# Optimization experiments

Hardware: AMD Instinct MI355X
Metric: run time of the kernel (lower is better)

Reference implementation:

```python
import jax, jax.numpy as jnp
import numpy as np
import math

B, S, D, H, TD = 256, 200, 64, 512, 8


def setup_inputs():
    key = jax.random.key(0)
    ks = jax.random.split(key, 12)
    sd, sh, so = 1.0 / math.sqrt(D), 1.0 / math.sqrt(H), 1.0 / math.sqrt(H + TD)
    return dict(
        x=jax.random.normal(ks[0], (B, S, D), jnp.float32),
        a=jax.random.normal(ks[3], (B, TD), jnp.float32),
        t=jnp.cumsum(jax.random.uniform(ks[2], (B, S), jnp.float32), axis=1),
        mask=(jax.random.uniform(ks[1], (B, S, D)) < 0.8).astype(jnp.float32),
        w_dg_x=jax.random.normal(ks[4], (D,), jnp.float32) * sd,
        b_dg_x=jnp.zeros((D,), jnp.float32),
        W_dg_h=jax.random.normal(ks[5], (H, D), jnp.float32) * sd,
        b_dg_h=jnp.zeros((H,), jnp.float32),
        W=jax.random.normal(ks[6], (3 * H, D), jnp.float32) * sd,
        U=jax.random.normal(ks[7], (3 * H, H), jnp.float32) * sh,
        V=jax.random.normal(ks[8], (3 * H, D), jnp.float32) * sd,
        b=jnp.zeros((3 * H,), jnp.float32),
        attn_v=jnp.ones((H,), jnp.float32),
        W_out=jax.random.normal(ks[9], (H, H + TD), jnp.float32) * so,
        b_out=jnp.zeros((H,), jnp.float32),
    )


def reference(x, a, t, mask, w_dg_x, b_dg_x, W_dg_h, b_dg_h, W, U, V, b, attn_v, W_out, b_out):
    # ---- GRU-D preprocessing: per-feature time gaps delta ----
    x_tm = jnp.transpose(x, (1, 0, 2))    # (S,B,D) time-major
    m_tm = jnp.transpose(mask, (1, 0, 2))
    dt = jnp.diff(t, axis=1, prepend=t[:, :1])      # (B,S), dt[0]=0
    dt_tm = jnp.transpose(dt)[:, :, None]           # (S,B,1)
    # delta[i] = dt[i] + (1 - mask[i-1]) * delta[i-1]; ones at step 0 -> delta[0]=0
    m_prev = jnp.concatenate([jnp.ones((1,) + m_tm.shape[1:], m_tm.dtype), m_tm[:-1]], axis=0)

    def delta_step(d, inp):
        dt_i, mp_i = inp
        d = dt_i + (1.0 - mp_i) * d
        return d, d

    _, delta_tm = jax.lax.scan(delta_step, jnp.zeros((B, D), x.dtype), (dt_tm, m_prev))

    # empirical mean of observed values for imputation
    x_mean = (mask * x).sum((0, 1)) / jnp.maximum(mask.sum((0, 1)), 1.0)  # (D,)

    Wz, Wr, Wh = W[:H], W[H:2 * H], W[2 * H:]
    Uz, Ur, Uh = U[:H], U[H:2 * H], U[2 * H:]
    Vz, Vr, Vh = V[:H], V[H:2 * H], V[2 * H:]
    bz, br, bh = b[:H], b[H:2 * H], b[2 * H:]

    def cell(carry, inp):
        h, x_last = carry
        x_i, m_i, d_i = inp                                        # (B,D) each
        gamma_x = jnp.exp(-jax.nn.relu(w_dg_x * d_i + b_dg_x))     # (B,D) input decay
        gamma_h = jnp.exp(-jax.nn.relu(d_i @ W_dg_h.T + b_dg_h))   # (B,H) hidden decay
        x_hat = m_i * x_i + (1.0 - m_i) * (gamma_x * x_last + (1.0 - gamma_x) * x_mean)
        h_dec = gamma_h * h
        z = jax.nn.sigmoid(x_hat @ Wz.T + h_dec @ Uz.T + m_i @ Vz.T + bz)
        r = jax.nn.sigmoid(x_hat @ Wr.T + h_dec @ Ur.T + m_i @ Vr.T + br)
        h_til = jnp.tanh(x_hat @ Wh.T + (r * h_dec) @ Uh.T + m_i @ Vh.T + bh)
        h_new = (1.0 - z) * h_dec + z * h_til
        x_last_new = m_i * x_i + (1.0 - m_i) * x_last
        return (h_new, x_last_new), h_new

    init = (jnp.zeros((B, H), x.dtype), jnp.zeros((B, D), x.dtype))
    _, h_all = jax.lax.scan(cell, init, (x_tm, m_tm, delta_tm))    # (S,B,H)

    # ---- attention pooling over time (softmax along seq dim, as in torch dim=0) ----
    score = (h_all @ attn_v) / math.sqrt(H)        # (S,B)
    w_attn = jax.nn.softmax(score, axis=0)
    attn_h = (h_all * w_attn[..., None]).sum(0)    # (B,H)

    # ---- treatment head ----
    return jnp.concatenate([attn_h, a], axis=1) @ W_out.T + b_out  # (B,H)
```

## Files before the change

### kernel.cpp

```cpp
#include <hip/hip_runtime.h>
#include <hip/hip_bf16.h>
#include <stdint.h>


typedef unsigned short u16;
typedef unsigned int   u32;
typedef unsigned long long u64;
typedef short bfrag  __attribute__((ext_vector_type(8)));
typedef u16   u16x8  __attribute__((ext_vector_type(8)));
typedef float f32x4  __attribute__((ext_vector_type(4)));

#define NB 256
#define NS 200
#define ND 64
#define NH 512

union UQ  { u16x8 h; bfrag s; u64 u[2]; uint4 q; };
union UF2 { float f[2]; u64 u; };

__device__ __forceinline__ float b2f(u16 v){ union { float f; u32 u; } c; c.u = ((u32)v) << 16; return c.f; }
__device__ __forceinline__ u16 f2b(float f){ union { float f; u32 u; } c; c.f = f; u32 r = c.u + 0x7FFFu + ((c.u >> 16) & 1u); return (u16)(r >> 16); }
__device__ __forceinline__ float sigm(float x){ return 1.f / (1.f + __expf(-x)); }
__device__ __forceinline__ float tanh_f(float x){ return 1.f - 2.f / (1.f + __expf(2.f * x)); }

__device__ __forceinline__ u64 cload64(const void* p){
  return __hip_atomic_load((const u64*)p, __ATOMIC_RELAXED, __HIP_MEMORY_SCOPE_AGENT);
}
__device__ __forceinline__ void cstore64(void* p, u64 v){
  __hip_atomic_store((u64*)p, v, __ATOMIC_RELAXED, __HIP_MEMORY_SCOPE_AGENT);
}
__device__ __forceinline__ void load8f_c(const float* p, float* f){
  UF2 w;
  w.u = cload64(p + 0); f[0]=w.f[0]; f[1]=w.f[1];
  w.u = cload64(p + 2); f[2]=w.f[0]; f[3]=w.f[1];
  w.u = cload64(p + 4); f[4]=w.f[0]; f[5]=w.f[1];
  w.u = cload64(p + 6); f[6]=w.f[0]; f[7]=w.f[1];
}
__device__ __forceinline__ void store8f_c(float* p, const float* f){
  UF2 w;
  w.f[0]=f[0]; w.f[1]=f[1]; cstore64(p + 0, w.u);
  w.f[0]=f[2]; w.f[1]=f[3]; cstore64(p + 2, w.u);
  w.f[0]=f[4]; w.f[1]=f[5]; cstore64(p + 4, w.u);
  w.f[0]=f[6]; w.f[1]=f[7]; cstore64(p + 6, w.u);
}
__device__ __forceinline__ void spin_ge(u32* f, u32 tgt){
  while (__hip_atomic_load(f, __ATOMIC_RELAXED, __HIP_MEMORY_SCOPE_AGENT) < tgt)
    __builtin_amdgcn_s_sleep(2);
}
__device__ __forceinline__ bfrag ldfrag(const float* src){
  f32x4 lo = *(const f32x4*)src;
  f32x4 hi = *(const f32x4*)(src + 4);
  UQ z;
  z.h[0]=f2b(lo[0]); z.h[1]=f2b(lo[1]); z.h[2]=f2b(lo[2]); z.h[3]=f2b(lo[3]);
  z.h[4]=f2b(hi[0]); z.h[5]=f2b(hi[1]); z.h[6]=f2b(hi[2]); z.h[7]=f2b(hi[3]);
  return z.s;
}


__global__ void transpose_k(const float* __restrict__ Wout, float* __restrict__ WT){
  int i = blockIdx.x * 256 + threadIdx.x;
  if (i < 520 * 512) { int k = i >> 9, ho = i & 511; WT[i] = Wout[ho * 520 + k]; }
}

__global__ void mean1_k(const float* __restrict__ x, const float* __restrict__ mask,
                        float* __restrict__ PX, float* __restrict__ PM){
  int s = blockIdx.x, tid = threadIdx.x;
  __shared__ float lx[256], lm[256];
  float xa = 0.f, ma = 0.f;
  for (int i = tid; i < NB * ND; i += 256) {
    int b = i >> 6, d = i & 63;
    size_t ix = ((size_t)b * NS + s) * 64 + d;
    float m = mask[ix];
    xa += m * x[ix]; ma += m;
  }
  lx[tid] = xa; lm[tid] = ma;
  __syncthreads();
  if (tid < 64) {
    PX[(size_t)s * 64 + tid] = lx[tid] + lx[tid + 64] + lx[tid + 128] + lx[tid + 192];
    PM[(size_t)s * 64 + tid] = lm[tid] + lm[tid + 64] + lm[tid + 128] + lm[tid + 192];
  }
}

__global__ void mean2_k(const float* __restrict__ PX, const float* __restrict__ PM,
                        float* __restrict__ XMEAN){
  int d = threadIdx.x;
  float sx = 0.f, sm = 0.f;
  for (int s = 0; s < NS; ++s){ sx += PX[s * 64 + d]; sm += PM[s * 64 + d]; }
  XMEAN[d] = sx / fmaxf(sm, 1.f);
}

__global__ void prep_k(const float* __restrict__ x, const float* __restrict__ mask,
                       const float* __restrict__ tc, const float* __restrict__ wdgx,
                       const float* __restrict__ bdgx, const float* __restrict__ XMEAN,
                       u16* __restrict__ XHAT, u16* __restrict__ MASKB, u16* __restrict__ DELTA){
  int g = blockIdx.x * 256 + threadIdx.x;
  int b = g >> 6, d = g & 63;
  float xmean = XMEAN[d], wx = wdgx[d], bx = bdgx[d];
  float xl = 0.f, del = 0.f, tprev = 0.f, mprev = 1.f;
  for (int s = 0; s < NS; ++s){
    float tv = tc[b * NS + s];
    float dtv = (s == 0) ? 0.f : (tv - tprev);
    tprev = tv;
    del = dtv + (1.f - mprev) * del;
    size_t ix = ((size_t)b * NS + s) * 64 + d;
    float m = mask[ix], xv = x[ix];
    float gx = __expf(-fmaxf(0.f, wx * del + bx));
    float xh = m * xv + (1.f - m) * (gx * xl + (1.f - gx) * xmean);
    size_t ox = ((size_t)s * NB + b) * 64 + d;
    XHAT[ox] = f2b(xh); MASKB[ox] = f2b(m); DELTA[ox] = f2b(del);
    xl = m * xv + (1.f - m) * xl;
    mprev = m;
  }
}

__global__ __launch_bounds__(256, 1) void grud_rnn(
    const float* __restrict__ Um, const float* __restrict__ Wm, const float* __restrict__ Vm,
    const float* __restrict__ bv, const float* __restrict__ Wdg, const float* __restrict__ bdg,
    const u16* __restrict__ XHAT, const u16* __restrict__ MASKB, const u16* __restrict__ DELTA,
    float* __restrict__ HDEC, u16* __restrict__ RHD, float* __restrict__ ZB,
    float* __restrict__ SHP, u16* __restrict__ HALL, u32* done1, u32* done2)
{
  const int tid = threadIdx.x, lane = tid & 63, wid = tid >> 6, bid = blockIdx.x;
  __shared__ u16 panel[80 * 16 * 8];
  __shared__ u16 dpanel[8 * 16 * 8];
  __shared__ float xpose[4][528];
  float* xp = xpose[wid];
  const int r = lane >> 2, cb = (lane & 3) * 8;
  const int krow = lane >> 4;

  if (bid < 192) {
    const int rb = bid / 12, sg = bid % 12;
    const int type = (sg < 4) ? 0 : ((sg < 8) ? 1 : 2);
    const int st = sg * 4 + wid;
    const int cglob = st * 32;
    const int m0 = rb * 16;
    const int c0 = cglob + (lane & 15);

    bfrag Bf[20][2];
    #pragma unroll
    for (int kk = 0; kk < 20; ++kk) {
      if (!(type == 2 && kk < 16)) {
        const int k0 = kk * 32 + krow * 8;
        #pragma unroll
        for (int t2 = 0; t2 < 2; ++t2) {
          const int c = c0 + t2 * 16;
          const float* src;
          if (k0 < 512)      src = Um + (size_t)c * 512 + k0;
          else if (k0 < 576) src = Wm + (size_t)c * 64 + (k0 - 512);
          else               src = Vm + (size_t)c * 64 + (k0 - 576);
          Bf[kk][t2] = ldfrag(src);
        }
      }
    }
    const float bias0 = bv[c0], bias1 = bv[c0 + 16];

    for (int t = 0; t < NS; ++t) {
      {
        const int isrc = tid >> 7, row = (tid >> 3) & 15, kb8 = tid & 7;
        const u16* sp = (isrc ? MASKB : XHAT) + ((size_t)t * NB + (m0 + row)) * 64 + kb8 * 8;
        uint4 vv = *(const uint4*)sp;
        *(uint4*)&panel[(((isrc ? 72 : 64) + kb8) * 16 + row) * 8] = vv;
      }
      if (tid == 0) spin_ge(done2 + rb * 16, 4u * (u32)t);
      __syncthreads();
      if (type != 2) {
        #pragma unroll
        for (int it = 0; it < 4; ++it) {
          const int c = it * 256 + tid;
          const int row = c >> 6, kb = c & 63;
          float f[8];
          load8f_c(HDEC + (size_t)(m0 + row) * 512 + kb * 8, f);
          UQ pv;
          #pragma unroll
          for (int j = 0; j < 8; ++j) pv.h[j] = f2b(f[j]);
          *(u16x8*)&panel[(kb * 16 + row) * 8] = pv.h;
        }
      }
      __syncthreads();
      f32x4 acc0 = {bias0, bias0, bias0, bias0};
      f32x4 acc1 = {bias1, bias1, bias1, bias1};
      #pragma unroll
      for (int kk = 0; kk < 20; ++kk) {
        if (!(type == 2 && kk < 16)) {
          bfrag a = *(const bfrag*)&panel[((kk * 4 + krow) * 16 + (lane & 15)) * 8];
          acc0 = __builtin_amdgcn_mfma_f32_16x16x32_bf16(a, Bf[kk][0], acc0, 0, 0, 0);
          acc1 = __builtin_amdgcn_mfma_f32_16x16x32_bf16(a, Bf[kk][1], acc1, 0, 0, 0);
        }
      }
      {
        const int r0 = krow * 4, cc = lane & 15;
        #pragma unroll
        for (int j = 0; j < 4; ++j) { xp[(r0 + j) * 33 + cc] = acc0[j]; xp[(r0 + j) * 33 + 16 + cc] = acc1[j]; }
      }
      float s8[8];
      #pragma unroll
      for (int q = 0; q < 8; ++q) s8[q] = xp[r * 33 + cb + q];
      const size_t orow = (size_t)(m0 + r) * 512;
      if (type == 0) {
        float zf[8];
        #pragma unroll
        for (int q = 0; q < 8; ++q) zf[q] = sigm(s8[q]);
        store8f_c(ZB + orow + cglob + cb, zf);
      } else if (type == 1) {
        const int hc = cglob - 512 + cb;
        UQ hv; hv.h = *(const u16x8*)&panel[((hc >> 3) * 16 + r) * 8];
        UQ pv;
        #pragma unroll
        for (int q = 0; q < 8; ++q) pv.h[q] = f2b(sigm(s8[q]) * b2f(hv.h[q]));
        u16* dst = RHD + orow + hc;
        cstore64(dst, pv.u[0]); cstore64(dst + 4, pv.u[1]);
      } else {
        store8f_c(SHP + orow + (cglob - 1024) + cb, s8);
      }
      asm volatile("s_waitcnt vmcnt(0)" ::: "memory");
      __syncthreads();
      if (tid == 0) __hip_atomic_fetch_add(done1 + rb * 16, 1u, __ATOMIC_RELAXED, __HIP_MEMORY_SCOPE_AGENT);
    }
  } else {
    const int b2 = bid - 192;
    const int rb = b2 >> 2, sg = b2 & 3;
    const int st = sg * 4 + wid;
    const int n0 = st * 32;
    const int m0 = rb * 16;
    const int c0 = n0 + (lane & 15);

    bfrag Bh[16][2];
    #pragma unroll
    for (int kk = 0; kk < 16; ++kk) {
      const int k0 = kk * 32 + krow * 8;
      #pragma unroll
      for (int t2 = 0; t2 < 2; ++t2)
        Bh[kk][t2] = ldfrag(Um + (size_t)(1024 + c0 + t2 * 16) * 512 + k0);
    }
    bfrag Bg[2][2];
    #pragma unroll
    for (int kk = 0; kk < 2; ++kk) {
      const int k0 = kk * 32 + krow * 8;
      #pragma unroll
      for (int t2 = 0; t2 < 2; ++t2)
        Bg[kk][t2] = ldfrag(Wdg + (size_t)(c0 + t2 * 16) * 64 + k0);
    }
    const float gb0 = bdg[c0], gb1 = bdg[c0 + 16];

    for (int t = 0; t < NS; ++t) {
      float gam[8] = {0,0,0,0,0,0,0,0};
      if (t < NS - 1) {
        if (tid < 128) {
          const int row = (tid >> 3) & 15, kb8 = tid & 7;
          const u16* sp = DELTA + ((size_t)(t + 1) * NB + (m0 + row)) * 64 + kb8 * 8;
          *(uint4*)&dpanel[(kb8 * 16 + row) * 8] = *(const uint4*)sp;
        }
        __syncthreads();
        f32x4 g0 = {gb0, gb0, gb0, gb0};
        f32x4 g1 = {gb1, gb1, gb1, gb1};
        #pragma unroll
        for (int kk = 0; kk < 2; ++kk) {
          bfrag a = *(const bfrag*)&dpanel[((kk * 4 + krow) * 16 + (lane & 15)) * 8];
          g0 = __builtin_amdgcn_mfma_f32_16x16x32_bf16(a, Bg[kk][0], g0, 0, 0, 0);
          g1 = __builtin_amdgcn_mfma_f32_16x16x32_bf16(a, Bg[kk][1], g1, 0, 0, 0);
        }
        const int r0 = krow * 4, cc = lane & 15;
        #pragma unroll
        for (int j = 0; j < 4; ++j) { xp[(r0 + j) * 33 + cc] = g0[j]; xp[(r0 + j) * 33 + 16 + cc] = g1[j]; }
        #pragma unroll
        for (int q = 0; q < 8; ++q) gam[q] = __expf(-fmaxf(0.f, xp[r * 33 + cb + q]));
      }
      if (tid == 0) spin_ge(done1 + rb * 16, 12u * (u32)(t + 1));
      __syncthreads();
      #pragma unroll
      for (int it = 0; it < 4; ++it) {
        const int c = it * 256 + tid;
        const int row = c >> 6, kb = c & 63;
        const u16* sp = RHD + (size_t)(m0 + row) * 512 + kb * 8;
        UQ pv; pv.u[0] = cload64(sp); pv.u[1] = cload64(sp + 4);
        *(u16x8*)&panel[(kb * 16 + row) * 8] = pv.h;
      }
      __syncthreads();
      f32x4 acc0 = {0.f, 0.f, 0.f, 0.f}, acc1 = {0.f, 0.f, 0.f, 0.f};
      #pragma unroll
      for (int kk = 0; kk < 16; ++kk) {
        bfrag a = *(const bfrag*)&panel[((kk * 4 + krow) * 16 + (lane & 15)) * 8];
        acc0 = __builtin_amdgcn_mfma_f32_16x16x32_bf16(a, Bh[kk][0], acc0, 0, 0, 0);
        acc1 = __builtin_amdgcn_mfma_f32_16x16x32_bf16(a, Bh[kk][1], acc1, 0, 0, 0);
      }
      {
        const int r0 = krow * 4, cc = lane & 15;
        #pragma unroll
        for (int j = 0; j < 4; ++j) { xp[(r0 + j) * 33 + cc] = acc0[j]; xp[(r0 + j) * 33 + 16 + cc] = acc1[j]; }
      }
      const int hc = n0 + cb;
      const size_t orow = (size_t)(m0 + r) * 512;
      float s2[8], shp[8], zz[8], hd[8], hn[8], hdn[8];
      #pragma unroll
      for (int q = 0; q < 8; ++q) s2[q] = xp[r * 33 + cb + q];
      load8f_c(SHP + orow + hc, shp);
      load8f_c(ZB + orow + hc, zz);
      load8f_c(HDEC + orow + hc, hd);
      UQ hw;
      #pragma unroll
      for (int q = 0; q < 8; ++q) {
        float til = tanh_f(shp[q] + s2[q]);
        hn[q] = (1.f - zz[q]) * hd[q] + zz[q] * til;
        hw.h[q] = f2b(hn[q]);
        hdn[q] = gam[q] * hn[q];
      }
      u16* hp = HALL + ((size_t)t * NB + (m0 + r)) * 512 + hc;
      cstore64(hp, hw.u[0]); cstore64(hp + 4, hw.u[1]);
      if (t < NS - 1) store8f_c(HDEC + orow + hc, hdn);
      asm volatile("s_waitcnt vmcnt(0)" ::: "memory");
      __syncthreads();
      if (tid == 0) __hip_atomic_fetch_add(done2 + rb * 16, 1u, __ATOMIC_RELAXED, __HIP_MEMORY_SCOPE_AGENT);
    }
  }
}


__global__ void attn_k(const u16* __restrict__ HALL, const float* __restrict__ av,
                       float* __restrict__ ATTN){
  const int b = blockIdx.x, tid = threadIdx.x, lane = tid & 63, wid = tid >> 6;
  __shared__ float avs[512], wgt[256], red[8];
  for (int i = tid; i < 512; i += 256) avs[i] = av[i];
  __syncthreads();
  float val = -3.0e38f;
  if (tid < NS) {
    const u16* hp = HALL + ((size_t)tid * NB + b) * 512;
    float acc = 0.f;
    for (int h = 0; h < 512; h += 8) {
      UQ w; w.q = *(const uint4*)(hp + h);
      #pragma unroll
      for (int j = 0; j < 8; ++j) acc += b2f(w.h[j]) * avs[h + j];
    }
    val = acc * 0.04419417382415922f;
  }
  float m = val;
  #pragma unroll
  for (int off = 32; off; off >>= 1) m = fmaxf(m, __shfl_xor(m, off, 64));
  if (lane == 0) red[wid] = m;
  __syncthreads();
  m = fmaxf(fmaxf(red[0], red[1]), fmaxf(red[2], red[3]));
  float e = (tid < NS) ? __expf(val - m) : 0.f;
  float sum = e;
  #pragma unroll
  for (int off = 32; off; off >>= 1) sum += __shfl_xor(sum, off, 64);
  if (lane == 0) red[4 + wid] = sum;
  __syncthreads();
  const float ssum = red[4] + red[5] + red[6] + red[7];
  wgt[tid] = e / ssum;
  __syncthreads();
  float a0 = 0.f, a1 = 0.f;
  const int h0 = tid * 2;
  for (int s = 0; s < NS; ++s) {
    float w = wgt[s];
    u32 pr = *(const u32*)(HALL + ((size_t)s * NB + b) * 512 + h0);
    a0 += w * b2f((u16)(pr & 0xFFFFu));
    a1 += w * b2f((u16)(pr >> 16));
  }
  ATTN[(size_t)b * 512 + h0] = a0;
  ATTN[(size_t)b * 512 + h0 + 1] = a1;
}

__global__ void out_k(const float* __restrict__ ATTN, const float* __restrict__ Ain,
                      const float* __restrict__ WT, const float* __restrict__ bout,
                      float* __restrict__ OUT){
  const int b = blockIdx.x, tid = threadIdx.x;
  __shared__ float ah[512], aa[8];
  for (int i = tid; i < 512; i += 256) ah[i] = ATTN[(size_t)b * 512 + i];
  if (tid < 8) aa[tid] = Ain[b * 8 + tid];
  __syncthreads();
  #pragma unroll
  for (int part = 0; part < 2; ++part) {
    const int ho = part * 256 + tid;
    float acc = bout[ho];
    #pragma unroll 8
    for (int k = 0; k < 512; ++k) acc += ah[k] * WT[(size_t)k * 512 + ho];
    #pragma unroll
    for (int k = 0; k < 8; ++k) acc += aa[k] * WT[(size_t)(512 + k) * 512 + ho];
    OUT[(size_t)b * 512 + ho] = acc;
  }
}


extern "C" void kernel_launch(void* const* d_in, const int* in_sizes, int n_in,
                              void* d_out, int out_size, void* d_ws, size_t ws_size,
                              hipStream_t stream) {
  (void)in_sizes; (void)n_in; (void)out_size; (void)ws_size;
  const float* x    = (const float*)d_in[0];
  const float* a_in = (const float*)d_in[1];
  const float* tc   = (const float*)d_in[2];
  const float* mask = (const float*)d_in[3];
  const float* wdgx = (const float*)d_in[4];
  const float* bdgx = (const float*)d_in[5];
  const float* Wdgh = (const float*)d_in[6];
  const float* bdgh = (const float*)d_in[7];
  const float* Wm   = (const float*)d_in[8];
  const float* Um   = (const float*)d_in[9];
  const float* Vm   = (const float*)d_in[10];
  const float* bvv  = (const float*)d_in[11];
  const float* attv = (const float*)d_in[12];
  const float* Wout = (const float*)d_in[13];
  const float* bout = (const float*)d_in[14];

  char* ws = (char*)d_ws;
  size_t o = 0;
  auto al = [&](size_t sz) { size_t r = o; o += (sz + 255) & ~(size_t)255; return r; };
  u32*   flags = (u32*)  (ws + al(4096));
  float* XMEAN = (float*)(ws + al(256));
  float* PX    = (float*)(ws + al((size_t)NS * 64 * 4));
  float* PM    = (float*)(ws + al((size_t)NS * 64 * 4));
  u16*   XHAT  = (u16*)  (ws + al((size_t)NS * NB * 64 * 2));
  u16*   MASKB = (u16*)  (ws + al((size_t)NS * NB * 64 * 2));
  u16*   DELTA = (u16*)  (ws + al((size_t)NS * NB * 64 * 2));
  float* HDEC  = (float*)(ws + al((size_t)NB * NH * 4));
  u16*   RHD   = (u16*)  (ws + al((size_t)NB * NH * 2));
  float* ZB    = (float*)(ws + al((size_t)NB * NH * 4));
  float* SHP   = (float*)(ws + al((size_t)NB * NH * 4));
  u16*   HALL  = (u16*)  (ws + al((size_t)NS * NB * NH * 2));
  float* ATTN  = (float*)(ws + al((size_t)NB * NH * 4));
  float* WT    = (float*)(ws + al((size_t)520 * 512 * 4));
  u32* done1 = flags;
  u32* done2 = flags + 256;

  hipMemsetAsync(flags, 0, 4096, stream);
  hipMemsetAsync(HDEC, 0, (size_t)NB * NH * 4, stream);

  transpose_k<<<(520 * 512 + 255) / 256, 256, 0, stream>>>(Wout, WT);
  mean1_k<<<NS, 256, 0, stream>>>(x, mask, PX, PM);
  mean2_k<<<1, 64, 0, stream>>>(PX, PM, XMEAN);
  prep_k<<<NB * ND / 256, 256, 0, stream>>>(x, mask, tc, wdgx, bdgx, XMEAN, XHAT, MASKB, DELTA);
  grud_rnn<<<256, 256, 0, stream>>>(Um, Wm, Vm, bvv, Wdgh, bdgh, XHAT, MASKB, DELTA,
                                    HDEC, RHD, ZB, SHP, HALL, done1, done2);
  attn_k<<<NB, 256, 0, stream>>>(HALL, attv, ATTN);
  out_k<<<NB, 256, 0, stream>>>(ATTN, a_in, WT, bout, (float*)d_out);
}
```

Before: 2.266 ms.

## Restructure GRU-D recurrence into pipelined hidden, input-projection and decay roles

The persistent RNN kernel is reorganised into 112 blocks per 16-row batch tile with three roles. Four blocks hold all U gate weights and run the recurrent matmuls. Two blocks precompute input and mask projections one step ahead into double-buffered bf16 slots. One block precomputes hidden-decay gammas ahead. Hidden state and r*h exchanges move from fp32 to bf16, and the spin waits now have bounded fuel with an abort flag. out_k is also batched over four rows per block to reuse W_out loads. The aim is to take the non-recurrent matmuls off the serial critical path, at the cost of more fine-grained flag synchronisation per step and a new intra-step barrier between the r and h-tilde phases.

```diff
diff --git a/kernel.cpp b/kernel.cpp
--- a/kernel.cpp
+++ b/kernel.cpp
@@ -15,6 +15,8 @@
 #define ND 64
 #define NH 512
 
+#define MFMA(a,b,c) __builtin_amdgcn_mfma_f32_16x16x32_bf16((a),(b),(c),0,0,0)
+
 union UQ  { u16x8 h; bfrag s; u64 u[2]; uint4 q; };
 union UF2 { float f[2]; u64 u; };
 
@@ -29,23 +31,16 @@
 __device__ __forceinline__ void cstore64(void* p, u64 v){
   __hip_atomic_store((u64*)p, v, __ATOMIC_RELAXED, __HIP_MEMORY_SCOPE_AGENT);
 }
-__device__ __forceinline__ void load8f_c(const float* p, float* f){
-  UF2 w;
-  w.u = cload64(p + 0); f[0]=w.f[0]; f[1]=w.f[1];
-  w.u = cload64(p + 2); f[2]=w.f[0]; f[3]=w.f[1];
-  w.u = cload64(p + 4); f[4]=w.f[0]; f[5]=w.f[1];
-  w.u = cload64(p + 6); f[6]=w.f[0]; f[7]=w.f[1];
-}
-__device__ __forceinline__ void store8f_c(float* p, const float* f){
-  UF2 w;
-  w.f[0]=f[0]; w.f[1]=f[1]; cstore64(p + 0, w.u);
-  w.f[0]=f[2]; w.f[1]=f[3]; cstore64(p + 2, w.u);
-  w.f[0]=f[4]; w.f[1]=f[5]; cstore64(p + 4, w.u);
-  w.f[0]=f[6]; w.f[1]=f[7]; cstore64(p + 6, w.u);
-}
-__device__ __forceinline__ void spin_ge(u32* f, u32 tgt){
-  while (__hip_atomic_load(f, __ATOMIC_RELAXED, __HIP_MEMORY_SCOPE_AGENT) < tgt)
-    __builtin_amdgcn_s_sleep(2);
+__device__ __forceinline__ bool spin_ge(u32* f, u32 tgt){
+  int fuel = 1 << 19;
+  while (__hip_atomic_load(f, __ATOMIC_RELAXED, __HIP_MEMORY_SCOPE_AGENT) < tgt) {
+    __builtin_amdgcn_s_sleep(1);
+    if (--fuel == 0) return false;
+  }
+  return true;
+}
+__device__ __forceinline__ void flag_add(u32* f){
+  __hip_atomic_fetch_add(f, 1u, __ATOMIC_RELAXED, __HIP_MEMORY_SCOPE_AGENT);
 }
 __device__ __forceinline__ bfrag ldfrag(const float* src){
   f32x4 lo = *(const f32x4*)src;
@@ -117,199 +112,242 @@
     const float* __restrict__ Um, const float* __restrict__ Wm, const float* __restrict__ Vm,
     const float* __restrict__ bv, const float* __restrict__ Wdg, const float* __restrict__ bdg,
     const u16* __restrict__ XHAT, const u16* __restrict__ MASKB, const u16* __restrict__ DELTA,
-    float* __restrict__ HDEC, u16* __restrict__ RHD, float* __restrict__ ZB,
-    float* __restrict__ SHP, u16* __restrict__ HALL, u32* done1, u32* done2)
+    u16* __restrict__ HDECB, u16* __restrict__ RHB, u16* __restrict__ XPART,
+    u16* __restrict__ GAMB, u16* __restrict__ HALL, u32* __restrict__ flags)
 {
   const int tid = threadIdx.x, lane = tid & 63, wid = tid >> 6, bid = blockIdx.x;
-  __shared__ u16 panel[80 * 16 * 8];
-  __shared__ u16 dpanel[8 * 16 * 8];
-  __shared__ float xpose[4][528];
-  float* xp = xpose[wid];
-  const int r = lane >> 2, cb = (lane & 3) * 8;
-  const int krow = lane >> 4;
-
-  if (bid < 192) {
-    const int rb = bid / 12, sg = bid % 12;
-    const int type = (sg < 4) ? 0 : ((sg < 8) ? 1 : 2);
-    const int st = sg * 4 + wid;
-    const int cglob = st * 32;
-    const int m0 = rb * 16;
-    const int c0 = cglob + (lane & 15);
-
-    bfrag Bf[20][2];
-    #pragma unroll
-    for (int kk = 0; kk < 20; ++kk) {
-      if (!(type == 2 && kk < 16)) {
-        const int k0 = kk * 32 + krow * 8;
-        #pragma unroll
-        for (int t2 = 0; t2 < 2; ++t2) {
-          const int c = c0 + t2 * 16;
-          const float* src;
-          if (k0 < 512)      src = Um + (size_t)c * 512 + k0;
-          else if (k0 < 576) src = Wm + (size_t)c * 64 + (k0 - 512);
-          else               src = Vm + (size_t)c * 64 + (k0 - 576);
-          Bf[kk][t2] = ldfrag(src);
-        }
-      }
-    }
-    const float bias0 = bv[c0], bias1 = bv[c0 + 16];
-
-    for (int t = 0; t < NS; ++t) {
-      {
-        const int isrc = tid >> 7, row = (tid >> 3) & 15, kb8 = tid & 7;
-        const u16* sp = (isrc ? MASKB : XHAT) + ((size_t)t * NB + (m0 + row)) * 64 + kb8 * 8;
-        uint4 vv = *(const uint4*)sp;
-        *(uint4*)&panel[(((isrc ? 72 : 64) + kb8) * 16 + row) * 8] = vv;
-      }
-      if (tid == 0) spin_ge(done2 + rb * 16, 4u * (u32)t);
-      __syncthreads();
-      if (type != 2) {
-        #pragma unroll
-        for (int it = 0; it < 4; ++it) {
-          const int c = it * 256 + tid;
-          const int row = c >> 6, kb = c & 63;
-          float f[8];
-          load8f_c(HDEC + (size_t)(m0 + row) * 512 + kb * 8, f);
-          UQ pv;
-          #pragma unroll
-          for (int j = 0; j < 8; ++j) pv.h[j] = f2b(f[j]);
-          *(u16x8*)&panel[(kb * 16 + row) * 8] = pv.h;
-        }
-      }
-      __syncthreads();
-      f32x4 acc0 = {bias0, bias0, bias0, bias0};
-      f32x4 acc1 = {bias1, bias1, bias1, bias1};
-      #pragma unroll
-      for (int kk = 0; kk < 20; ++kk) {
-        if (!(type == 2 && kk < 16)) {
-          bfrag a = *(const bfrag*)&panel[((kk * 4 + krow) * 16 + (lane & 15)) * 8];
-          acc0 = __builtin_amdgcn_mfma_f32_16x16x32_bf16(a, Bf[kk][0], acc0, 0, 0, 0);
-          acc1 = __builtin_amdgcn_mfma_f32_16x16x32_bf16(a, Bf[kk][1], acc1, 0, 0, 0);
-        }
-      }
-      {
-        const int r0 = krow * 4, cc = lane & 15;
-        #pragma unroll
-        for (int j = 0; j < 4; ++j) { xp[(r0 + j) * 33 + cc] = acc0[j]; xp[(r0 + j) * 33 + 16 + cc] = acc1[j]; }
-      }
-      float s8[8];
-      #pragma unroll
-      for (int q = 0; q < 8; ++q) s8[q] = xp[r * 33 + cb + q];
-      const size_t orow = (size_t)(m0 + r) * 512;
-      if (type == 0) {
-        float zf[8];
-        #pragma unroll
-        for (int q = 0; q < 8; ++q) zf[q] = sigm(s8[q]);
-        store8f_c(ZB + orow + cglob + cb, zf);
-      } else if (type == 1) {
-        const int hc = cglob - 512 + cb;
-        UQ hv; hv.h = *(const u16x8*)&panel[((hc >> 3) * 16 + r) * 8];
-        UQ pv;
-        #pragma unroll
-        for (int q = 0; q < 8; ++q) pv.h[q] = f2b(sigm(s8[q]) * b2f(hv.h[q]));
-        u16* dst = RHD + orow + hc;
-        cstore64(dst, pv.u[0]); cstore64(dst + 4, pv.u[1]);
-      } else {
-        store8f_c(SHP + orow + (cglob - 1024) + cb, s8);
-      }
-      asm volatile("s_waitcnt vmcnt(0)" ::: "memory");
-      __syncthreads();
-      if (tid == 0) __hip_atomic_fetch_add(done1 + rb * 16, 1u, __ATOMIC_RELAXED, __HIP_MEMORY_SCOPE_AGENT);
-    }
-  } else {
-    const int b2 = bid - 192;
-    const int rb = b2 >> 2, sg = b2 & 3;
-    const int st = sg * 4 + wid;
-    const int n0 = st * 32;
-    const int m0 = rb * 16;
-    const int c0 = n0 + (lane & 15);
-
-    bfrag Bh[16][2];
+  const int rb = bid / 7, role = bid % 7, m0 = rb * 16;
+  const int l16 = lane & 15, krow = lane >> 4, r4 = lane >> 2, cb = (lane & 3) * 8;
+  u32* FH = flags + rb * 128;
+  u32* FR = flags + rb * 128 + 32;
+  u32* FX = flags + rb * 128 + 64;
+  u32* FG = flags + rb * 128 + 96;
+
+  __shared__ u16 hpanel[64 * 16 * 8];
+  __shared__ u16 rhpanel[64 * 16 * 8];
+  __shared__ float xb[4][16 * 33];
+  __shared__ int s_ab;
+  float* xw = xb[wid];
+  const f32x4 Z4 = {0.f, 0.f, 0.f, 0.f};
+  if (tid == 0) s_ab = 0;
+  __syncthreads();
+
+  if (role < 4) {
+    const int c0g = role * 128 + wid * 32;
+    bfrag BUz[16][2], BUr[16][2], BUh[16][2];
     #pragma unroll
     for (int kk = 0; kk < 16; ++kk) {
-      const int k0 = kk * 32 + krow * 8;
-      #pragma unroll
-      for (int t2 = 0; t2 < 2; ++t2)
-        Bh[kk][t2] = ldfrag(Um + (size_t)(1024 + c0 + t2 * 16) * 512 + k0);
-    }
-    bfrag Bg[2][2];
+      #pragma unroll
+      for (int t2 = 0; t2 < 2; ++t2) {
+        const size_t ko = (size_t)(kk * 32 + krow * 8);
+        BUz[kk][t2] = ldfrag(Um + (size_t)(       c0g + t2 * 16 + l16) * 512 + ko);
+        BUr[kk][t2] = ldfrag(Um + (size_t)(512  + c0g + t2 * 16 + l16) * 512 + ko);
+        BUh[kk][t2] = ldfrag(Um + (size_t)(1024 + c0g + t2 * 16 + l16) * 512 + ko);
+      }
+    }
+
+    for (int t = 0; t < NS; ++t) {
+      const int slot = t & 1;
+      if (tid == 0 && t > 0)  { if (!spin_ge(FH, 4u * (u32)t)) s_ab = 1; }
+      if (tid == 64)          { if (!spin_ge(FX, 2u * (u32)(t + 1))) s_ab = 1; }
+      if (tid == 128)         { u32 gt = (t + 1 < NS) ? (u32)(t + 1) : (u32)(NS - 1);
+                                if (!spin_ge(FG, gt)) s_ab = 1; }
+      __syncthreads();
+      if (s_ab) break;
+      const u16* xpb = XPART + (((size_t)slot * 16 + rb) * 16 + r4) * 1536;
+      u64 xz0 = cload64(xpb + c0g + cb),        xz1 = cload64(xpb + c0g + cb + 4);
+      u64 xr0 = cload64(xpb + 512 + c0g + cb),  xr1 = cload64(xpb + 512 + c0g + cb + 4);
+      u64 xh0 = cload64(xpb + 1024 + c0g + cb), xh1 = cload64(xpb + 1024 + c0g + cb + 4);
+      u64 gm0 = 0, gm1 = 0;
+      if (t + 1 < NS) {
+        const u16* gpb = GAMB + (((size_t)((t + 1) & 1) * 16 + rb) * 16 + r4) * 512 + c0g + cb;
+        gm0 = cload64(gpb); gm1 = cload64(gpb + 4);
+      }
+      {
+        const int srow = tid >> 4, sc = (tid & 15) * 32;
+        u16* dp = &hpanel[((sc >> 3) * 16 + srow) * 8];
+        if (t > 0) {
+          const u16* hs = HDECB + (size_t)(m0 + srow) * 512 + sc;
+          u64 a0 = cload64(hs),      a1 = cload64(hs + 4),  a2 = cload64(hs + 8),  a3 = cload64(hs + 12);
+          u64 a4 = cload64(hs + 16), a5 = cload64(hs + 20), a6 = cload64(hs + 24), a7 = cload64(hs + 28);
+          *(u64*)(dp)       = a0; *(u64*)(dp + 4)   = a1;
+          *(u64*)(dp + 128) = a2; *(u64*)(dp + 132) = a3;
+          *(u64*)(dp + 256) = a4; *(u64*)(dp + 260) = a5;
+          *(u64*)(dp + 384) = a6; *(u64*)(dp + 388) = a7;
+        } else {
+          *(u64*)(dp)       = 0; *(u64*)(dp + 4)   = 0;
+          *(u64*)(dp + 128) = 0; *(u64*)(dp + 132) = 0;
+          *(u64*)(dp + 256) = 0; *(u64*)(dp + 260) = 0;
+          *(u64*)(dp + 384) = 0; *(u64*)(dp + 388) = 0;
+        }
+      }
+      __syncthreads();
+      f32x4 ar0 = Z4, ar1 = Z4;
+      #pragma unroll
+      for (int kk = 0; kk < 16; ++kk) {
+        bfrag a = *(const bfrag*)&hpanel[((kk * 4 + krow) * 16 + l16) * 8];
+        ar0 = MFMA(a, BUr[kk][0], ar0); ar1 = MFMA(a, BUr[kk][1], ar1);
+      }
+      #pragma unroll
+      for (int j = 0; j < 4; ++j) { xw[(krow*4+j)*33 + l16] = ar0[j]; xw[(krow*4+j)*33 + 16 + l16] = ar1[j]; }
+      UQ xru; xru.u[0] = xr0; xru.u[1] = xr1;
+      UQ hdu; hdu.h = *(const u16x8*)&hpanel[(((c0g + cb) >> 3) * 16 + r4) * 8];
+      UQ rhv;
+      #pragma unroll
+      for (int q = 0; q < 8; ++q) {
+        float rv = sigm(b2f(xru.h[q]) + xw[r4 * 33 + cb + q]);
+        rhv.h[q] = f2b(rv * b2f(hdu.h[q]));
+      }
+      { u16* dst = RHB + (size_t)(m0 + r4) * 512 + c0g + cb;
+        cstore64(dst, rhv.u[0]); cstore64(dst + 4, rhv.u[1]); }
+      asm volatile("s_waitcnt vmcnt(0)" ::: "memory");
+      __syncthreads();
+      if (tid == 0) flag_add(FR);
+      f32x4 az0 = Z4, az1 = Z4;
+      #pragma unroll
+      for (int kk = 0; kk < 16; ++kk) {
+        bfrag a = *(const bfrag*)&hpanel[((kk * 4 + krow) * 16 + l16) * 8];
+        az0 = MFMA(a, BUz[kk][0], az0); az1 = MFMA(a, BUz[kk][1], az1);
+      }
+      #pragma unroll
+      for (int j = 0; j < 4; ++j) { xw[(krow*4+j)*33 + l16] = az0[j]; xw[(krow*4+j)*33 + 16 + l16] = az1[j]; }
+      UQ xzu; xzu.u[0] = xz0; xzu.u[1] = xz1;
+      float zz8[8];
+      #pragma unroll
+      for (int q = 0; q < 8; ++q) zz8[q] = sigm(b2f(xzu.h[q]) + xw[r4 * 33 + cb + q]);
+      if (tid == 0) { if (!spin_ge(FR, 4u * (u32)(t + 1))) s_ab = 1; }
+      __syncthreads();
+      if (s_ab) break;
+      {
+        const int srow = tid >> 4, sc = (tid & 15) * 32;
+        const u16* rs = RHB + (size_t)(m0 + srow) * 512 + sc;
+        u64 a0 = cload64(rs),      a1 = cload64(rs + 4),  a2 = cload64(rs + 8),  a3 = cload64(rs + 12);
+        u64 a4 = cload64(rs + 16), a5 = cload64(rs + 20), a6 = cload64(rs + 24), a7 = cload64(rs + 28);
+        u16* dp = &rhpanel[((sc >> 3) * 16 + srow) * 8];
+        *(u64*)(dp)       = a0; *(u64*)(dp + 4)   = a1;
+        *(u64*)(dp + 128) = a2; *(u64*)(dp + 132) = a3;
+        *(u64*)(dp + 256) = a4; *(u64*)(dp + 260) = a5;
+        *(u64*)(dp + 384) = a6; *(u64*)(dp + 388) = a7;
+      }
+      __syncthreads();
+      f32x4 ah0 = Z4, ah1 = Z4;
+      #pragma unroll
+      for (int kk = 0; kk < 16; ++kk) {
+        bfrag a = *(const bfrag*)&rhpanel[((kk * 4 + krow) * 16 + l16) * 8];
+        ah0 = MFMA(a, BUh[kk][0], ah0); ah1 = MFMA(a, BUh[kk][1], ah1);
+      }
+      #pragma unroll
+      for (int j = 0; j < 4; ++j) { xw[(krow*4+j)*33 + l16] = ah0[j]; xw[(krow*4+j)*33 + 16 + l16] = ah1[j]; }
+      UQ xhu; xhu.u[0] = xh0; xhu.u[1] = xh1;
+      UQ hwv; float hn8[8];
+      #pragma unroll
+      for (int q = 0; q < 8; ++q) {
+        float til = tanh_f(b2f(xhu.h[q]) + xw[r4 * 33 + cb + q]);
+        float hdq = b2f(hdu.h[q]);
+        float hv = (1.f - zz8[q]) * hdq + zz8[q] * til;
+        hn8[q] = hv; hwv.h[q] = f2b(hv);
+      }
+      if (t + 1 < NS) {
+        UQ gmu; gmu.u[0] = gm0; gmu.u[1] = gm1;
+        UQ hdn;
+        #pragma unroll
+        for (int q = 0; q < 8; ++q) hdn.h[q] = f2b(b2f(gmu.h[q]) * hn8[q]);
+        u16* dp2 = HDECB + (size_t)(m0 + r4) * 512 + c0g + cb;
+        cstore64(dp2, hdn.u[0]); cstore64(dp2 + 4, hdn.u[1]);
+      }
+      asm volatile("s_waitcnt vmcnt(0)" ::: "memory");
+      __syncthreads();
+      if (tid == 0) flag_add(FH);
+      *(uint4*)(HALL + ((size_t)t * NB + m0 + r4) * 512 + c0g + cb) = hwv.q;
+    }
+  } else if (role < 6) {
+    const int p = role - 4;
+    const int wbase = p * 768 + wid * 192;
+    bfrag BW[12][2], BV2[12][2];
     #pragma unroll
-    for (int kk = 0; kk < 2; ++kk) {
-      const int k0 = kk * 32 + krow * 8;
-      #pragma unroll
-      for (int t2 = 0; t2 < 2; ++t2)
-        Bg[kk][t2] = ldfrag(Wdg + (size_t)(c0 + t2 * 16) * 64 + k0);
-    }
-    const float gb0 = bdg[c0], gb1 = bdg[c0 + 16];
+    for (int ct = 0; ct < 12; ++ct)
+      #pragma unroll
+      for (int kx = 0; kx < 2; ++kx) {
+        BW[ct][kx]  = ldfrag(Wm + (size_t)(wbase + ct * 16 + l16) * 64 + kx * 32 + krow * 8);
+        BV2[ct][kx] = ldfrag(Vm + (size_t)(wbase + ct * 16 + l16) * 64 + kx * 32 + krow * 8);
+      }
+    float bias6[6][8];
+    #pragma unroll
+    for (int grp = 0; grp < 6; ++grp)
+      #pragma unroll
+      for (int q = 0; q < 8; ++q) bias6[grp][q] = bv[wbase + grp * 32 + cb + q];
 
     for (int t = 0; t < NS; ++t) {
-      float gam[8] = {0,0,0,0,0,0,0,0};
-      if (t < NS - 1) {
-        if (tid < 128) {
-          const int row = (tid >> 3) & 15, kb8 = tid & 7;
-          const u16* sp = DELTA + ((size_t)(t + 1) * NB + (m0 + row)) * 64 + kb8 * 8;
-          *(uint4*)&dpanel[(kb8 * 16 + row) * 8] = *(const uint4*)sp;
+      if (tid == 0 && t >= 2) { if (!spin_ge(FH, 4u * (u32)(t - 1))) s_ab = 1; }
+      { const int kb = tid >> 4, row = tid & 15;
+        const u16* sp = (kb < 8 ? XHAT : MASKB) + ((size_t)t * NB + m0 + row) * 64 + (kb & 7) * 8;
+        *(uint4*)&hpanel[(kb * 16 + row) * 8] = *(const uint4*)sp; }
+      __syncthreads();
+      if (s_ab) break;
+      u16* orow_ = XPART + (((size_t)(t & 1) * 16 + rb) * 16 + r4) * 1536 + wbase;
+      #pragma unroll
+      for (int grp = 0; grp < 6; ++grp) {
+        f32x4 ac0 = Z4, ac1 = Z4;
+        #pragma unroll
+        for (int kx = 0; kx < 2; ++kx) {
+          bfrag ax = *(const bfrag*)&hpanel[((kx * 4 + krow) * 16 + l16) * 8];
+          ac0 = MFMA(ax, BW[grp*2][kx], ac0); ac1 = MFMA(ax, BW[grp*2+1][kx], ac1);
+          bfrag am = *(const bfrag*)&hpanel[((8 + kx * 4 + krow) * 16 + l16) * 8];
+          ac0 = MFMA(am, BV2[grp*2][kx], ac0); ac1 = MFMA(am, BV2[grp*2+1][kx], ac1);
         }
-        __syncthreads();
-        f32x4 g0 = {gb0, gb0, gb0, gb0};
-        f32x4 g1 = {gb1, gb1, gb1, gb1};
-        #pragma unroll
-        for (int kk = 0; kk < 2; ++kk) {
-          bfrag a = *(const bfrag*)&dpanel[((kk * 4 + krow) * 16 + (lane & 15)) * 8];
-          g0 = __builtin_amdgcn_mfma_f32_16x16x32_bf16(a, Bg[kk][0], g0, 0, 0, 0);
-          g1 = __builtin_amdgcn_mfma_f32_16x16x32_bf16(a, Bg[kk][1], g1, 0, 0, 0);
+        #pragma unroll
+        for (int j = 0; j < 4; ++j) { xw[(krow*4+j)*33 + l16] = ac0[j]; xw[(krow*4+j)*33 + 16 + l16] = ac1[j]; }
+        UQ ov;
+        #pragma unroll
+        for (int q = 0; q < 8; ++q) ov.h[q] = f2b(xw[r4 * 33 + cb + q] + bias6[grp][q]);
+        cstore64(orow_ + grp * 32 + cb, ov.u[0]); cstore64(orow_ + grp * 32 + cb + 4, ov.u[1]);
+      }
+      asm volatile("s_waitcnt vmcnt(0)" ::: "memory");
+      __syncthreads();
+      if (tid == 0) flag_add(FX);
+    }
+  } else {
+    bfrag BG[8][2];
+    #pragma unroll
+    for (int ct = 0; ct < 8; ++ct)
+      #pragma unroll
+      for (int kx = 0; kx < 2; ++kx)
+        BG[ct][kx] = ldfrag(Wdg + (size_t)(wid * 128 + ct * 16 + l16) * 64 + kx * 32 + krow * 8);
+    float gb4[4][8];
+    #pragma unroll
+    for (int grp = 0; grp < 4; ++grp)
+      #pragma unroll
+      for (int q = 0; q < 8; ++q) gb4[grp][q] = bdg[wid * 128 + grp * 32 + cb + q];
+
+    for (int tt = 1; tt < NS; ++tt) {
+      if (tid == 0 && tt >= 3) { if (!spin_ge(FH, 4u * (u32)(tt - 2))) s_ab = 1; }
+      if (tid < 128) {
+        const int kb = tid >> 4, row = tid & 15;
+        const u16* sp = DELTA + ((size_t)tt * NB + m0 + row) * 64 + kb * 8;
+        *(uint4*)&hpanel[(kb * 16 + row) * 8] = *(const uint4*)sp;
+      }
+      __syncthreads();
+      if (s_ab) break;
+      u16* orow_ = GAMB + (((size_t)(tt & 1) * 16 + rb) * 16 + r4) * 512 + wid * 128;
+      #pragma unroll
+      for (int grp = 0; grp < 4; ++grp) {
+        f32x4 ac0 = Z4, ac1 = Z4;
+        #pragma unroll
+        for (int kx = 0; kx < 2; ++kx) {
+          bfrag a = *(const bfrag*)&hpanel[((kx * 4 + krow) * 16 + l16) * 8];
+          ac0 = MFMA(a, BG[grp*2][kx], ac0); ac1 = MFMA(a, BG[grp*2+1][kx], ac1);
         }
-        const int r0 = krow * 4, cc = lane & 15;
-        #pragma unroll
-        for (int j = 0; j < 4; ++j) { xp[(r0 + j) * 33 + cc] = g0[j]; xp[(r0 + j) * 33 + 16 + cc] = g1[j]; }
-        #pragma unroll
-        for (int q = 0; q < 8; ++q) gam[q] = __expf(-fmaxf(0.f, xp[r * 33 + cb + q]));
-      }
-      if (tid == 0) spin_ge(done1 + rb * 16, 12u * (u32)(t + 1));
-      __syncthreads();
-      #pragma unroll
-      for (int it = 0; it < 4; ++it) {
-        const int c = it * 256 + tid;
-        const int row = c >> 6, kb = c & 63;
-        const u16* sp = RHD + (size_t)(m0 + row) * 512 + kb * 8;
-        UQ pv; pv.u[0] = cload64(sp); pv.u[1] = cload64(sp + 4);
-        *(u16x8*)&panel[(kb * 16 + row) * 8] = pv.h;
-      }
-      __syncthreads();
-      f32x4 acc0 = {0.f, 0.f, 0.f, 0.f}, acc1 = {0.f, 0.f, 0.f, 0.f};
-      #pragma unroll
-      for (int kk = 0; kk < 16; ++kk) {
-        bfrag a = *(const bfrag*)&panel[((kk * 4 + krow) * 16 + (lane & 15)) * 8];
-        acc0 = __builtin_amdgcn_mfma_f32_16x16x32_bf16(a, Bh[kk][0], acc0, 0, 0, 0);
-        acc1 = __builtin_amdgcn_mfma_f32_16x16x32_bf16(a, Bh[kk][1], acc1, 0, 0, 0);
-      }
-      {
-        const int r0 = krow * 4, cc = lane & 15;
-        #pragma unroll
-        for (int j = 0; j < 4; ++j) { xp[(r0 + j) * 33 + cc] = acc0[j]; xp[(r0 + j) * 33 + 16 + cc] = acc1[j]; }
-      }
-      const int hc = n0 + cb;
-      const size_t orow = (size_t)(m0 + r) * 512;
-      float s2[8], shp[8], zz[8], hd[8], hn[8], hdn[8];
-      #pragma unroll
-      for (int q = 0; q < 8; ++q) s2[q] = xp[r * 33 + cb + q];
-      load8f_c(SHP + orow + hc, shp);
-      load8f_c(ZB + orow + hc, zz);
-      load8f_c(HDEC + orow + hc, hd);
-      UQ hw;
-      #pragma unroll
-      for (int q = 0; q < 8; ++q) {
-        float til = tanh_f(shp[q] + s2[q]);
-        hn[q] = (1.f - zz[q]) * hd[q] + zz[q] * til;
-        hw.h[q] = f2b(hn[q]);
-        hdn[q] = gam[q] * hn[q];
-      }
-      u16* hp = HALL + ((size_t)t * NB + (m0 + r)) * 512 + hc;
-      cstore64(hp, hw.u[0]); cstore64(hp + 4, hw.u[1]);
-      if (t < NS - 1) store8f_c(HDEC + orow + hc, hdn);
+        #pragma unroll
+        for (int j = 0; j < 4; ++j) { xw[(krow*4+j)*33 + l16] = ac0[j]; xw[(krow*4+j)*33 + 16 + l16] = ac1[j]; }
+        UQ ov;
+        #pragma unroll
+        for (int q = 0; q < 8; ++q)
+          ov.h[q] = f2b(__expf(-fmaxf(0.f, xw[r4 * 33 + cb + q] + gb4[grp][q])));
+        cstore64(orow_ + grp * 32 + cb, ov.u[0]); cstore64(orow_ + grp * 32 + cb + 4, ov.u[1]);
+      }
       asm volatile("s_waitcnt vmcnt(0)" ::: "memory");
       __syncthreads();
-      if (tid == 0) __hip_atomic_fetch_add(done2 + rb * 16, 1u, __ATOMIC_RELAXED, __HIP_MEMORY_SCOPE_AGENT);
+      if (tid == 0) flag_add(FG);
     }
   }
 }
@@ -362,20 +400,26 @@
 __global__ void out_k(const float* __restrict__ ATTN, const float* __restrict__ Ain,
                       const float* __restrict__ WT, const float* __restrict__ bout,
                       float* __restrict__ OUT){
-  const int b = blockIdx.x, tid = threadIdx.x;
-  __shared__ float ah[512], aa[8];
-  for (int i = tid; i < 512; i += 256) ah[i] = ATTN[(size_t)b * 512 + i];
-  if (tid < 8) aa[tid] = Ain[b * 8 + tid];
+  const int g = blockIdx.x, tid = threadIdx.x;
+  __shared__ float ah[4][520];
+  for (int i = tid; i < 4 * 520; i += 256) {
+    int bb = i / 520, k = i % 520;
+    int b = g * 4 + bb;
+    ah[bb][k] = (k < 512) ? ATTN[(size_t)b * 512 + k] : Ain[b * 8 + (k - 512)];
+  }
   __syncthreads();
   #pragma unroll
   for (int part = 0; part < 2; ++part) {
     const int ho = part * 256 + tid;
-    float acc = bout[ho];
-    #pragma unroll 8
-    for (int k = 0; k < 512; ++k) acc += ah[k] * WT[(size_t)k * 512 + ho];
-    #pragma unroll
-    for (int k = 0; k < 8; ++k) acc += aa[k] * WT[(size_t)(512 + k) * 512 + ho];
-    OUT[(size_t)b * 512 + ho] = acc;
+    float a0 = bout[ho], a1 = a0, a2 = a0, a3 = a0;
+    for (int k = 0; k < 520; ++k) {
+      float w = WT[(size_t)k * 512 + ho];
+      a0 += ah[0][k] * w; a1 += ah[1][k] * w; a2 += ah[2][k] * w; a3 += ah[3][k] * w;
+    }
+    OUT[(size_t)(g * 4 + 0) * 512 + ho] = a0;
+    OUT[(size_t)(g * 4 + 1) * 512 + ho] = a1;
+    OUT[(size_t)(g * 4 + 2) * 512 + ho] = a2;
+    OUT[(size_t)(g * 4 + 3) * 512 + ho] = a3;
   }
 }
 
@@ -403,32 +447,29 @@
   char* ws = (char*)d_ws;
   size_t o = 0;
   auto al = [&](size_t sz) { size_t r = o; o += (sz + 255) & ~(size_t)255; return r; };
-  u32*   flags = (u32*)  (ws + al(4096));
+  u32*   flags = (u32*)  (ws + al(16 * 128 * 4));
   float* XMEAN = (float*)(ws + al(256));
   float* PX    = (float*)(ws + al((size_t)NS * 64 * 4));
   float* PM    = (float*)(ws + al((size_t)NS * 64 * 4));
   u16*   XHAT  = (u16*)  (ws + al((size_t)NS * NB * 64 * 2));
   u16*   MASKB = (u16*)  (ws + al((size_t)NS * NB * 64 * 2));
   u16*   DELTA = (u16*)  (ws + al((size_t)NS * NB * 64 * 2));
-  float* HDEC  = (float*)(ws + al((size_t)NB * NH * 4));
-  u16*   RHD   = (u16*)  (ws + al((size_t)NB * NH * 2));
-  float* ZB    = (float*)(ws + al((size_t)NB * NH * 4));
-  float* SHP   = (float*)(ws + al((size_t)NB * NH * 4));
+  u16*   HDECB = (u16*)  (ws + al((size_t)NB * NH * 2));
+  u16*   RHB   = (u16*)  (ws + al((size_t)NB * NH * 2));
+  u16*   XPART = (u16*)  (ws + al((size_t)2 * 16 * 16 * 1536 * 2));
+  u16*   GAMB  = (u16*)  (ws + al((size_t)2 * 16 * 16 * 512 * 2));
   u16*   HALL  = (u16*)  (ws + al((size_t)NS * NB * NH * 2));
   float* ATTN  = (float*)(ws + al((size_t)NB * NH * 4));
   float* WT    = (float*)(ws + al((size_t)520 * 512 * 4));
-  u32* done1 = flags;
-  u32* done2 = flags + 256;
-
-  hipMemsetAsync(flags, 0, 4096, stream);
-  hipMemsetAsync(HDEC, 0, (size_t)NB * NH * 4, stream);
+
+  hipMemsetAsync(flags, 0, 16 * 128 * 4, stream);
 
   transpose_k<<<(520 * 512 + 255) / 256, 256, 0, stream>>>(Wout, WT);
   mean1_k<<<NS, 256, 0, stream>>>(x, mask, PX, PM);
   mean2_k<<<1, 64, 0, stream>>>(PX, PM, XMEAN);
   prep_k<<<NB * ND / 256, 256, 0, stream>>>(x, mask, tc, wdgx, bdgx, XMEAN, XHAT, MASKB, DELTA);
-  grud_rnn<<<256, 256, 0, stream>>>(Um, Wm, Vm, bvv, Wdgh, bdgh, XHAT, MASKB, DELTA,
-                                    HDEC, RHD, ZB, SHP, HALL, done1, done2);
+  grud_rnn<<<112, 256, 0, stream>>>(Um, Wm, Vm, bvv, Wdgh, bdgh, XHAT, MASKB, DELTA,
+                                    HDECB, RHB, XPART, GAMB, HALL, flags);
   attn_k<<<NB, 256, 0, stream>>>(HALL, attv, ATTN);
-  out_k<<<NB, 256, 0, stream>>>(ATTN, a_in, WT, bout, (float*)d_out);
-}
+  out_k<<<64, 256, 0, stream>>>(ATTN, a_in, WT, bout, (float*)d_out);
+}
```

Result: faster. 1.934 ms (-14.6%).
